# Optimization experiments

Measured on AMD Instinct MI355X. Metric: run time of the kernel, lower is better.

Reference implementation:

```python
import jax, jax.numpy as jnp
import numpy as np

VOCAB = 32000
BLOCK = 2048
C = 1024
H = 16
L = 4
D = C // H
B, T = 1, 2048


def setup_inputs() -> dict:
    key = jax.random.key(0)
    ks = jax.random.split(key, 16)
    s = 0.02
    inp = {
        "input_ids": jax.random.randint(ks[0], (B, T), 0, VOCAB),
        "wte": jax.random.normal(ks[1], (VOCAB, C), jnp.float32) * s,  # tied with lm_head
        "wpe": jax.random.normal(ks[2], (BLOCK, C), jnp.float32) * s,
        "ln1_w": jnp.ones((L, C), jnp.float32),
        "ln1_b": jnp.zeros((L, C), jnp.float32),
        "attn_w": jax.random.normal(ks[3], (L, 3 * C, C), jnp.float32) * s,
        "attn_b": jnp.zeros((L, 3 * C), jnp.float32),
        "proj_w": jax.random.normal(ks[4], (L, C, C), jnp.float32) * (s / np.sqrt(2 * L)),
        "proj_b": jnp.zeros((L, C), jnp.float32),
        "ln2_w": jnp.ones((L, C), jnp.float32),
        "ln2_b": jnp.zeros((L, C), jnp.float32),
        "fc_w": jax.random.normal(ks[5], (L, 4 * C, C), jnp.float32) * s,
        "fc_b": jnp.zeros((L, 4 * C), jnp.float32),
        "fcp_w": jax.random.normal(ks[6], (L, C, 4 * C), jnp.float32) * (s / np.sqrt(2 * L)),
        "fcp_b": jnp.zeros((L, C), jnp.float32),
        "lnf_w": jnp.ones((C,), jnp.float32),
        "lnf_b": jnp.zeros((C,), jnp.float32),
    }
    return inp


def _layernorm(x, w, b, eps=1e-5):
    mu = jnp.mean(x, axis=-1, keepdims=True)
    var = jnp.mean(jnp.square(x - mu), axis=-1, keepdims=True)
    return (x - mu) * jax.lax.rsqrt(var + eps) * w + b


def _block(x, ln1_w, ln1_b, aw, ab, pw, pb, ln2_w, ln2_b, fw, fb, fpw, fpb):
    b, t, c = x.shape
    h = _layernorm(x, ln1_w, ln1_b)
    qkv = h @ aw.T + ab                      # (B,T,3C)
    q, k, v = jnp.split(qkv, 3, axis=-1)
    q = q.reshape(b, t, H, D)
    k = k.reshape(b, t, H, D)
    v = v.reshape(b, t, H, D)
    scale = 1.0 / np.sqrt(D)
    att = jnp.einsum("bqhd,bkhd->bhqk", q, k) * scale   # O(T^2) scores
    mask = jnp.tril(jnp.ones((t, t), bool))
    att = jnp.where(mask, att, -jnp.inf)
    att = jax.nn.softmax(att, axis=-1)
    y = jnp.einsum("bhqk,bkhd->bqhd", att, v).reshape(b, t, c)
    x = x + (y @ pw.T + pb)
    h = _layernorm(x, ln2_w, ln2_b)
    h = jax.nn.gelu(h @ fw.T + fb, approximate=False)
    x = x + (h @ fpw.T + fpb)
    return x


def reference(input_ids, wte, wpe, ln1_w, ln1_b, attn_w, attn_b, proj_w, proj_b,
              ln2_w, ln2_b, fc_w, fc_b, fcp_w, fcp_b, lnf_w, lnf_b):
    b, t = input_ids.shape
    x = wte[input_ids] + wpe[:t]             # (B,T,C)
    for l in range(L):
        x = _block(x, ln1_w[l], ln1_b[l], attn_w[l], attn_b[l], proj_w[l], proj_b[l],
                   ln2_w[l], ln2_b[l], fc_w[l], fc_b[l], fcp_w[l], fcp_b[l])
    x = _layernorm(x, lnf_w, lnf_b)
    logits = x @ wte.T                        # tied lm_head, no bias
    return logits
```

## Files before the change

### kernel.cpp

```cpp
#include <hip/hip_runtime.h>
#include <hip/hip_bf16.h>
#include <math.h>

#define TT 2048
#define CC 1024
#define HH 16
#define DD 64
#define LL 4
#define VOCAB_N 32000

using bf16 = __hip_bfloat16;
typedef __bf16 bf16x8 __attribute__((ext_vector_type(8)));
typedef float f32x4 __attribute__((ext_vector_type(4)));

typedef unsigned int uint_gl __attribute__((address_space(1)));
typedef unsigned int uint_ld __attribute__((address_space(3)));

__device__ __forceinline__ void gload_lds16(const bf16* g, bf16* l) {
    __builtin_amdgcn_global_load_lds((const uint_gl*)g, (uint_ld*)l, 16, 0, 0);
}

__global__ __launch_bounds__(256) void embed_kernel(const int* __restrict__ ids,
                                                    const float* __restrict__ wte,
                                                    const float* __restrict__ wpe,
                                                    float* __restrict__ x) {
    int t = blockIdx.x;
    int id = ids[t];
    int tid = threadIdx.x;
    float4 a = ((const float4*)(wte + (size_t)id * CC))[tid];
    float4 p = ((const float4*)(wpe + (size_t)t * CC))[tid];
    a.x += p.x; a.y += p.y; a.z += p.z; a.w += p.w;
    ((float4*)(x + (size_t)t * CC))[tid] = a;
}

__global__ __launch_bounds__(256) void ln_kernel(const float* __restrict__ x,
                                                 const float* __restrict__ w,
                                                 const float* __restrict__ b,
                                                 bf16* __restrict__ out) {
    int row = blockIdx.x;
    int tid = threadIdx.x;
    const float* xr = x + (size_t)row * CC;
    float4 v = ((const float4*)xr)[tid];
    float s = v.x + v.y + v.z + v.w;
    float ss = v.x * v.x + v.y * v.y + v.z * v.z + v.w * v.w;
    #pragma unroll
    for (int off = 32; off > 0; off >>= 1) {
        s += __shfl_down(s, off, 64);
        ss += __shfl_down(ss, off, 64);
    }
    __shared__ float sbuf[8];
    int wv = tid >> 6;
    if ((tid & 63) == 0) { sbuf[wv] = s; sbuf[4 + wv] = ss; }
    __syncthreads();
    s = sbuf[0] + sbuf[1] + sbuf[2] + sbuf[3];
    ss = sbuf[4] + sbuf[5] + sbuf[6] + sbuf[7];
    float mu = s * (1.0f / CC);
    float var = ss * (1.0f / CC) - mu * mu;
    float rs = rsqrtf(var + 1e-5f);
    float4 wv4 = ((const float4*)w)[tid];
    float4 bv4 = ((const float4*)b)[tid];
    size_t base = (size_t)row * CC + tid * 4;
    out[base + 0] = __float2bfloat16((v.x - mu) * rs * wv4.x + bv4.x);
    out[base + 1] = __float2bfloat16((v.y - mu) * rs * wv4.y + bv4.y);
    out[base + 2] = __float2bfloat16((v.z - mu) * rs * wv4.z + bv4.z);
    out[base + 3] = __float2bfloat16((v.w - mu) * rs * wv4.w + bv4.w);
}

__global__ __launch_bounds__(256) void cvt_kernel(const float* __restrict__ in,
                                                  bf16* __restrict__ out, int n) {
    int i = (blockIdx.x * 256 + threadIdx.x) * 4;
    if (i < n) {
        float4 v = *(const float4*)(in + i);
        out[i + 0] = __float2bfloat16(v.x);
        out[i + 1] = __float2bfloat16(v.y);
        out[i + 2] = __float2bfloat16(v.z);
        out[i + 3] = __float2bfloat16(v.w);
    }
}

template <int EPI, int KSPLIT>
__global__ __launch_bounds__(256) void gemm_bt(const bf16* __restrict__ A,
                                               const bf16* __restrict__ W,
                                               const float* __restrict__ bias,
                                               bf16* __restrict__ outb,
                                               float* __restrict__ outf,
                                               int M, int N, int K) {
    __shared__ bf16 At[128 * 32];
    __shared__ bf16 Bt[128 * 32];
    const int tid = threadIdx.x;
    const int wv = tid >> 6;
    const int ln = tid & 15;
    const int quad = (tid & 63) >> 4;
    const int wm = (wv >> 1) * 64;
    const int wn = (wv & 1) * 64;

    const int gx = gridDim.x, gy = gridDim.y;
    int f = blockIdx.y * gx + blockIdx.x;
    int nfull = gx >> 4;
    int fullB = nfull * 16 * gy;
    int bx, by;
    if (f < fullB) {
        int p = f / (16 * gy);
        int r = f - p * (16 * gy);
        bx = p * 16 + (r & 15);
        by = r >> 4;
    } else {
        int r = f - fullB;
        int w = gx - (nfull << 4);
        bx = (nfull << 4) + r % w;
        by = r / w;
    }
    const int m0 = by * 128;
    const int n0 = bx * 128;
    const int kb = K / KSPLIT;
    const int k_beg = (KSPLIT > 1) ? blockIdx.z * kb : 0;
    const int k_end = k_beg + kb;

    f32x4 acc[4][4];
    #pragma unroll
    for (int i = 0; i < 4; i++)
        #pragma unroll
        for (int j = 0; j < 4; j++)
            #pragma unroll
            for (int r = 0; r < 4; r++) acc[i][j][r] = 0.0f;

    const int rsw = (ln >> 1) & 3;

    for (int k0 = k_beg; k0 < k_end; k0 += 32) {
        #pragma unroll
        for (int r = 0; r < 2; r++) {
            int ci = r * 256 + tid;
            int row = ci >> 2;
            int lc = (ci & 3) ^ ((row >> 1) & 3);
            gload_lds16(A + (size_t)(m0 + row) * K + k0 + lc * 8,
                        At + (size_t)(r * 256 + wv * 64) * 8);
            gload_lds16(W + (size_t)(n0 + row) * K + k0 + lc * 8,
                        Bt + (size_t)(r * 256 + wv * 64) * 8);
        }
        __syncthreads();
        bf16x8 af[4], bfg[4];
        #pragma unroll
        for (int i = 0; i < 4; i++)
            af[i] = *(const bf16x8*)&At[(wm + i * 16 + ln) * 32 + (quad ^ rsw) * 8];
        #pragma unroll
        for (int j = 0; j < 4; j++)
            bfg[j] = *(const bf16x8*)&Bt[(wn + j * 16 + ln) * 32 + (quad ^ rsw) * 8];
        #pragma unroll
        for (int i = 0; i < 4; i++)
            #pragma unroll
            for (int j = 0; j < 4; j++)
                acc[i][j] = __builtin_amdgcn_mfma_f32_16x16x32_bf16(af[i], bfg[j], acc[i][j], 0, 0, 0);
        __syncthreads();
    }

    const bool addBias = (EPI != 3) && (KSPLIT == 1 || blockIdx.z == 0);
    #pragma unroll
    for (int j = 0; j < 4; j++) {
        int col = n0 + wn + j * 16 + ln;
        float bv = addBias ? bias[col] : 0.0f;
        #pragma unroll
        for (int i = 0; i < 4; i++) {
            int rowb = m0 + wm + i * 16 + quad * 4;
            #pragma unroll
            for (int r = 0; r < 4; r++) {
                float v = acc[i][j][r] + bv;
                size_t idx = (size_t)(rowb + r) * N + col;
                if (EPI == 0) {
                    outb[idx] = __float2bfloat16(v);
                } else if (EPI == 1) {
                    outb[idx] = __float2bfloat16(0.5f * v * (1.0f + erff(v * 0.70710678118654752f)));
                } else if (EPI == 2) {
                    if (KSPLIT > 1) atomicAdd(&outf[idx], v);
                    else outf[idx] += v;
                } else {
                    outf[idx] = v;
                }
            }
        }
    }
}

__global__ __launch_bounds__(256) void vtrans_kernel(const bf16* __restrict__ qkv,
                                                     bf16* __restrict__ vT) {
    const int h = blockIdx.x;
    const int t0 = blockIdx.y * 64;
    __shared__ __bf16 tl[64][72];
    const int tid = threadIdx.x;
    const int rhalf = tid >> 3;
    const int c8 = (tid & 7) * 8;
    #pragma unroll
    for (int rr = 0; rr < 2; rr++) {
        int row = rhalf + 32 * rr;
        bf16x8 v = *(const bf16x8*)(qkv + (size_t)(t0 + row) * (3 * CC) + 2 * CC + h * DD + c8);
        #pragma unroll
        for (int i = 0; i < 8; i++) tl[c8 + i][row] = v[i];
    }
    __syncthreads();
    #pragma unroll
    for (int rr = 0; rr < 2; rr++) {
        int d = rhalf + 32 * rr;
        bf16x8 o;
        #pragma unroll
        for (int i = 0; i < 8; i++) o[i] = tl[d][c8 + i];
        *(bf16x8*)(vT + (size_t)(h * DD + d) * TT + t0 + c8) = o;
    }
}

__global__ __launch_bounds__(256) void attn_kernel(const bf16* __restrict__ qkv,
                                                   const bf16* __restrict__ vT,
                                                   bf16* __restrict__ y) {
    const int h = blockIdx.x;
    const int q0 = blockIdx.y * 128;
    const int tid = threadIdx.x;
    const int wq = tid >> 6;
    const int ln = tid & 15;
    const int quad = (tid & 63) >> 4;
    const int wr0 = q0 + wq * 32;

    __shared__ bf16 Kt[64 * 64];
    __shared__ bf16 Vt[64 * 64];
    __shared__ bf16 Pt[4][32 * 72];

    bf16x8 qf[2][2];
    #pragma unroll
    for (int qi = 0; qi < 2; qi++)
        #pragma unroll
        for (int ks = 0; ks < 2; ks++)
            qf[qi][ks] = *(const bf16x8*)(qkv + (size_t)(wr0 + qi * 16 + ln) * (3 * CC) + h * DD + ks * 32 + quad * 8);

    f32x4 oy[2][4];
    float mrow[2], lrow[2];
    #pragma unroll
    for (int i = 0; i < 2; i++) {
        #pragma unroll
        for (int j = 0; j < 4; j++)
            #pragma unroll
            for (int r = 0; r < 4; r++) oy[i][j][r] = 0.0f;
        mrow[i] = -INFINITY;
        lrow[i] = 0.0f;
    }

    const int ntiles = q0 / 64 + 2;
    for (int kt = 0; kt < ntiles; kt++) {
        const int kt0 = kt * 64;
        #pragma unroll
        for (int r = 0; r < 2; r++) {
            int ci = r * 256 + tid;
            int row = ci >> 3;
            int lc = (ci & 7) ^ (row & 7);
            gload_lds16(qkv + (size_t)(kt0 + row) * (3 * CC) + CC + h * DD + lc * 8,
                        Kt + (size_t)(r * 256 + wq * 64) * 8);
            gload_lds16(vT + (size_t)(h * DD + row) * TT + kt0 + lc * 8,
                        Vt + (size_t)(r * 256 + wq * 64) * 8);
        }
        __syncthreads();

        if (kt0 <= wr0) {
            bf16x8 kf[4][2];
            #pragma unroll
            for (int ki = 0; ki < 4; ki++)
                #pragma unroll
                for (int ks = 0; ks < 2; ks++) {
                    int Rk = ki * 16 + ln;
                    kf[ki][ks] = *(const bf16x8*)&Kt[Rk * 64 + (((ks * 4 + quad) ^ (Rk & 7))) * 8];
                }
            f32x4 st[4][2];
            #pragma unroll
            for (int ki = 0; ki < 4; ki++)
                #pragma unroll
                for (int qi = 0; qi < 2; qi++)
                    #pragma unroll
                    for (int r = 0; r < 4; r++) st[ki][qi][r] = 0.0f;
            #pragma unroll
            for (int ks = 0; ks < 2; ks++)
                #pragma unroll
                for (int ki = 0; ki < 4; ki++)
                    #pragma unroll
                    for (int qi = 0; qi < 2; qi++)
                        st[ki][qi] = __builtin_amdgcn_mfma_f32_16x16x32_bf16(kf[ki][ks], qf[qi][ks], st[ki][qi], 0, 0, 0);

            const float scale = 0.125f;
            float alpha[2];
            #pragma unroll
            for (int qi = 0; qi < 2; qi++) {
                int q = wr0 + qi * 16 + ln;
                float sv[4][4];
                float mx = -INFINITY;
                #pragma unroll
                for (int ki = 0; ki < 4; ki++)
                    #pragma unroll
                    for (int r = 0; r < 4; r++) {
                        float t = st[ki][qi][r] * scale;
                        int key = kt0 + ki * 16 + quad * 4 + r;
                        if (key > q) t = -INFINITY;
                        sv[ki][r] = t;
                        mx = fmaxf(mx, t);
                    }
                mx = fmaxf(mx, __shfl_xor(mx, 16, 64));
                mx = fmaxf(mx, __shfl_xor(mx, 32, 64));
                float mnew = fmaxf(mrow[qi], mx);
                alpha[qi] = __expf(mrow[qi] - mnew);
                mrow[qi] = mnew;
                float ps = 0.0f;
                #pragma unroll
                for (int ki = 0; ki < 4; ki++)
                    #pragma unroll
                    for (int r = 0; r < 4; r++) {
                        float p = __expf(sv[ki][r] - mnew);
                        ps += p;
                        Pt[wq][(qi * 16 + ln) * 72 + ki * 16 + quad * 4 + r] = __float2bfloat16(p);
                    }
                ps += __shfl_xor(ps, 16, 64);
                ps += __shfl_xor(ps, 32, 64);
                lrow[qi] = lrow[qi] * alpha[qi] + ps;
            }

            #pragma unroll
            for (int i = 0; i < 2; i++)
                #pragma unroll
                for (int r = 0; r < 4; r++) {
                    float a = __shfl(alpha[i], quad * 4 + r, 16);
                    #pragma unroll
                    for (int dn = 0; dn < 4; dn++) oy[i][dn][r] *= a;
                }

            bf16x8 pf[2][2], vf[4][2];
            #pragma unroll
            for (int i = 0; i < 2; i++)
                #pragma unroll
                for (int ks = 0; ks < 2; ks++)
                    pf[i][ks] = *(const bf16x8*)&Pt[wq][(i * 16 + ln) * 72 + ks * 32 + quad * 8];
            #pragma unroll
            for (int dn = 0; dn < 4; dn++)
                #pragma unroll
                for (int ks = 0; ks < 2; ks++) {
                    int Rd = dn * 16 + ln;
                    vf[dn][ks] = *(const bf16x8*)&Vt[Rd * 64 + (((ks * 4 + quad) ^ (Rd & 7))) * 8];
                }
            #pragma unroll
            for (int ks = 0; ks < 2; ks++)
                #pragma unroll
                for (int i = 0; i < 2; i++)
                    #pragma unroll
                    for (int dn = 0; dn < 4; dn++)
                        oy[i][dn] = __builtin_amdgcn_mfma_f32_16x16x32_bf16(pf[i][ks], vf[dn][ks], oy[i][dn], 0, 0, 0);
        }
        __syncthreads();
    }

    #pragma unroll
    for (int i = 0; i < 2; i++)
        #pragma unroll
        for (int r = 0; r < 4; r++) {
            float linv = 1.0f / __shfl(lrow[i], quad * 4 + r, 16);
            int row = wr0 + i * 16 + quad * 4 + r;
            #pragma unroll
            for (int dn = 0; dn < 4; dn++)
                y[(size_t)row * CC + h * DD + dn * 16 + ln] = __float2bfloat16(oy[i][dn][r] * linv);
        }
}

extern "C" void kernel_launch(void* const* d_in, const int* in_sizes, int n_in,
                              void* d_out, int out_size, void* d_ws, size_t ws_size,
                              hipStream_t stream) {
    const int*   ids    = (const int*)d_in[0];
    const float* wte    = (const float*)d_in[1];
    const float* wpe    = (const float*)d_in[2];
    const float* ln1_w  = (const float*)d_in[3];
    const float* ln1_b  = (const float*)d_in[4];
    const float* attn_w = (const float*)d_in[5];
    const float* attn_b = (const float*)d_in[6];
    const float* proj_w = (const float*)d_in[7];
    const float* proj_b = (const float*)d_in[8];
    const float* ln2_w  = (const float*)d_in[9];
    const float* ln2_b  = (const float*)d_in[10];
    const float* fc_w   = (const float*)d_in[11];
    const float* fc_b   = (const float*)d_in[12];
    const float* fcp_w  = (const float*)d_in[13];
    const float* fcp_b  = (const float*)d_in[14];
    const float* lnf_w  = (const float*)d_in[15];
    const float* lnf_b  = (const float*)d_in[16];

    char* ws = (char*)d_ws;
    float* x    = (float*)(ws);
    bf16* hbuf  = (bf16*)(ws + 8388608);
    bf16* g4buf = (bf16*)(ws + 12582912);
    bf16* qkvb  = (bf16*)(ws + 29360128);
    bf16* ybuf  = (bf16*)(ws + 41943040);
    bf16* wbuf  = (bf16*)(ws + 46137344);
    bf16* vtb   = g4buf;

    embed_kernel<<<TT, 256, 0, stream>>>(ids, wte, wpe, x);

    for (int l = 0; l < LL; l++) {
        ln_kernel<<<TT, 256, 0, stream>>>(x, ln1_w + l * CC, ln1_b + l * CC, hbuf);

        cvt_kernel<<<(3 * CC * CC) / 1024, 256, 0, stream>>>(attn_w + (size_t)l * 3 * CC * CC, wbuf, 3 * CC * CC);
        gemm_bt<0, 1><<<dim3(3 * CC / 128, TT / 128), 256, 0, stream>>>(hbuf, wbuf, attn_b + l * 3 * CC,
                                                                        qkvb, nullptr, TT, 3 * CC, CC);

        vtrans_kernel<<<dim3(HH, TT / 64), 256, 0, stream>>>(qkvb, vtb);
        attn_kernel<<<dim3(HH, TT / 128), 256, 0, stream>>>(qkvb, vtb, ybuf);

        cvt_kernel<<<(CC * CC) / 1024, 256, 0, stream>>>(proj_w + (size_t)l * CC * CC, wbuf, CC * CC);
        gemm_bt<2, 2><<<dim3(CC / 128, TT / 128, 2), 256, 0, stream>>>(ybuf, wbuf, proj_b + l * CC,
                                                                       nullptr, x, TT, CC, CC);

        ln_kernel<<<TT, 256, 0, stream>>>(x, ln2_w + l * CC, ln2_b + l * CC, hbuf);

        cvt_kernel<<<(4 * CC * CC) / 1024, 256, 0, stream>>>(fc_w + (size_t)l * 4 * CC * CC, wbuf, 4 * CC * CC);
        gemm_bt<1, 1><<<dim3(4 * CC / 128, TT / 128), 256, 0, stream>>>(hbuf, wbuf, fc_b + l * 4 * CC,
                                                                        g4buf, nullptr, TT, 4 * CC, CC);

        cvt_kernel<<<(4 * CC * CC) / 1024, 256, 0, stream>>>(fcp_w + (size_t)l * 4 * CC * CC, wbuf, 4 * CC * CC);
        gemm_bt<2, 2><<<dim3(CC / 128, TT / 128, 2), 256, 0, stream>>>(g4buf, wbuf, fcp_b + l * CC,
                                                                       nullptr, x, TT, CC, 4 * CC);
    }

    ln_kernel<<<TT, 256, 0, stream>>>(x, lnf_w, lnf_b, hbuf);
    cvt_kernel<<<(VOCAB_N * CC) / 1024, 256, 0, stream>>>(wte, wbuf, VOCAB_N * CC);
    gemm_bt<3, 1><<<dim3(VOCAB_N / 128, TT / 128), 256, 0, stream>>>(hbuf, wbuf, nullptr,
                                                                     nullptr, (float*)d_out, TT, VOCAB_N, CC);
}
```

Baseline: 1.583 ms.

## Add 256x256 pipelined MFMA GEMM for lm_head and vectorize weight conversion

Replaces the 128x128 GEMM used for the large vocabulary projection with a new 256x256-tile, 512-thread kernel. The new kernel double-buffers LDS via direct global-to-LDS loads with XOR swizzle, interleaves staging with quarter-tile MFMA phases under s_setprio, and remaps workgroups for L2 locality. It also widens the fp32-to-bf16 weight conversion kernel to 8 elements per thread with a single vector store. The larger tiles raise data reuse on the dominant GEMM but use far more LDS and registers, and the hand-written waitcnt/barrier schedule is fragile.

```diff
diff --git a/kernel.cpp b/kernel.cpp
--- a/kernel.cpp
+++ b/kernel.cpp
@@ -19,6 +19,10 @@
 __device__ __forceinline__ void gload_lds16(const bf16* g, bf16* l) {
     __builtin_amdgcn_global_load_lds((const uint_gl*)g, (uint_ld*)l, 16, 0, 0);
 }
+
+#define VMCNT(n) asm volatile("s_waitcnt vmcnt(" #n ")" ::: "memory")
+#define MEMFENCE asm volatile("" ::: "memory")
+#define BAR() do { MEMFENCE; __builtin_amdgcn_s_barrier(); MEMFENCE; } while (0)
 
 __global__ __launch_bounds__(256) void embed_kernel(const int* __restrict__ ids,
                                                     const float* __restrict__ wte,
@@ -68,13 +72,20 @@
 
 __global__ __launch_bounds__(256) void cvt_kernel(const float* __restrict__ in,
                                                   bf16* __restrict__ out, int n) {
-    int i = (blockIdx.x * 256 + threadIdx.x) * 4;
+    int i = (blockIdx.x * 256 + threadIdx.x) * 8;
     if (i < n) {
-        float4 v = *(const float4*)(in + i);
-        out[i + 0] = __float2bfloat16(v.x);
-        out[i + 1] = __float2bfloat16(v.y);
-        out[i + 2] = __float2bfloat16(v.z);
-        out[i + 3] = __float2bfloat16(v.w);
+        float4 a = *(const float4*)(in + i);
+        float4 b = *(const float4*)(in + i + 4);
+        bf16 tmp[8];
+        tmp[0] = __float2bfloat16(a.x);
+        tmp[1] = __float2bfloat16(a.y);
+        tmp[2] = __float2bfloat16(a.z);
+        tmp[3] = __float2bfloat16(a.w);
+        tmp[4] = __float2bfloat16(b.x);
+        tmp[5] = __float2bfloat16(b.y);
+        tmp[6] = __float2bfloat16(b.z);
+        tmp[7] = __float2bfloat16(b.w);
+        *(bf16x8*)(out + i) = *(const bf16x8*)tmp;
     }
 }
 
@@ -178,6 +189,148 @@
             }
         }
     }
+}
+
+__device__ __forceinline__ void stage_q(const bf16* __restrict__ X, bf16* dst,
+                                        int r0, int K, int k0, int q, int tid) {
+    const int g = q * 512 + tid;
+    const int row = g >> 3;
+    const int lc = (g & 7) ^ (row & 7);
+    gload_lds16(X + (size_t)(r0 + row) * K + k0 + lc * 8,
+                dst + (size_t)(q * 512 + (tid & 0x1C0)) * 8);
+}
+
+template <int QI>
+__device__ __forceinline__ void rd_a(const bf16* Ab, int wm2, int ln, int quad, bf16x8 af[4][2]) {
+    #pragma unroll
+    for (int i = 0; i < 4; i++) {
+        const int row = wm2 * 128 + QI * 64 + i * 16 + ln;
+        #pragma unroll
+        for (int ks = 0; ks < 2; ks++)
+            af[i][ks] = *(const bf16x8*)&Ab[row * 64 + ((ks * 4 + quad) ^ (ln & 7)) * 8];
+    }
+}
+
+template <int QJ>
+__device__ __forceinline__ void rd_b(const bf16* Bb, int wn2, int ln, int quad, bf16x8 bfr[2][2]) {
+    #pragma unroll
+    for (int j = 0; j < 2; j++) {
+        const int row = wn2 * 64 + QJ * 32 + j * 16 + ln;
+        #pragma unroll
+        for (int ks = 0; ks < 2; ks++)
+            bfr[j][ks] = *(const bf16x8*)&Bb[row * 64 + ((ks * 4 + quad) ^ (ln & 7)) * 8];
+    }
+}
+
+template <int QI, int QJ>
+__device__ __forceinline__ void mfma_q(bf16x8 af[4][2], bf16x8 bfr[2][2], f32x4 acc[8][4]) {
+    __builtin_amdgcn_s_setprio(1);
+    #pragma unroll
+    for (int ks = 0; ks < 2; ks++)
+        #pragma unroll
+        for (int i = 0; i < 4; i++)
+            #pragma unroll
+            for (int j = 0; j < 2; j++)
+                acc[QI * 4 + i][QJ * 2 + j] =
+                    __builtin_amdgcn_mfma_f32_16x16x32_bf16(af[i][ks], bfr[j][ks],
+                                                            acc[QI * 4 + i][QJ * 2 + j], 0, 0, 0);
+    __builtin_amdgcn_s_setprio(0);
+}
+
+__global__ __launch_bounds__(512, 2) void gemm256(const bf16* __restrict__ A,
+                                                  const bf16* __restrict__ W,
+                                                  float* __restrict__ out,
+                                                  int M, int N, int K) {
+    __shared__ bf16 As[2][256 * 64];
+    __shared__ bf16 Bs[2][256 * 64];
+    const int tid = threadIdx.x;
+    const int ln = tid & 15;
+    const int quad = (tid & 63) >> 4;
+    const int wv = tid >> 6;
+    const int wm2 = wv >> 2;
+    const int wn2 = wv & 3;
+
+    const int cpx = gridDim.x >> 3;
+    const int wg = (blockIdx.x & 7) * cpx + (blockIdx.x >> 3);
+    const int byn = M >> 8;
+    const int bx = wg / byn;
+    const int by = wg - bx * byn;
+    const int m0 = by * 256;
+    const int n0 = bx * 256;
+
+    f32x4 acc[8][4];
+    #pragma unroll
+    for (int i = 0; i < 8; i++)
+        #pragma unroll
+        for (int j = 0; j < 4; j++)
+            #pragma unroll
+            for (int r = 0; r < 4; r++) acc[i][j][r] = 0.0f;
+
+    const int nt = K >> 6;
+
+    #pragma unroll
+    for (int q = 0; q < 4; q++) stage_q(A, As[0], m0, K, 0, q, tid);
+    #pragma unroll
+    for (int q = 0; q < 4; q++) stage_q(W, Bs[0], n0, K, 0, q, tid);
+    #pragma unroll
+    for (int q = 0; q < 4; q++) stage_q(A, As[1], m0, K, 64, q, tid);
+
+    for (int tt = 0; tt < nt; tt++) {
+        const int c = tt & 1;
+        const bf16* Ab = As[c];
+        const bf16* Bb = Bs[c];
+        bf16* An = As[c];
+        bf16* Bn = Bs[c ^ 1];
+
+        if (tt < nt - 1) { VMCNT(4); } else { VMCNT(0); }
+        __builtin_amdgcn_s_barrier();
+        MEMFENCE;
+
+        bf16x8 af[4][2], bfr[2][2];
+
+        if (tt + 1 < nt) {
+            #pragma unroll
+            for (int q = 0; q < 4; q++) stage_q(W, Bn, n0, K, (tt + 1) * 64, q, tid);
+        }
+        rd_a<0>(Ab, wm2, ln, quad, af);
+        rd_b<0>(Bb, wn2, ln, quad, bfr);
+        BAR();
+        mfma_q<0, 0>(af, bfr, acc);
+        BAR();
+
+        if (tt + 2 < nt) {
+            stage_q(A, An, m0, K, (tt + 2) * 64, 0, tid);
+            stage_q(A, An, m0, K, (tt + 2) * 64, 2, tid);
+        }
+        rd_b<1>(Bb, wn2, ln, quad, bfr);
+        BAR();
+        mfma_q<0, 1>(af, bfr, acc);
+        BAR();
+
+        rd_a<1>(Ab, wm2, ln, quad, af);
+        BAR();
+        mfma_q<1, 1>(af, bfr, acc);
+        BAR();
+
+        if (tt + 2 < nt) {
+            stage_q(A, An, m0, K, (tt + 2) * 64, 1, tid);
+            stage_q(A, An, m0, K, (tt + 2) * 64, 3, tid);
+        }
+        rd_b<0>(Bb, wn2, ln, quad, bfr);
+        BAR();
+        mfma_q<1, 0>(af, bfr, acc);
+    }
+
+    #pragma unroll
+    for (int gi = 0; gi < 8; gi++)
+        #pragma unroll
+        for (int gj = 0; gj < 4; gj++) {
+            const int rowb = m0 + wm2 * 128 + gi * 16 + quad * 4;
+            const int col = n0 + wn2 * 64 + gj * 16 + ln;
+            #pragma unroll
+            for (int r = 0; r < 4; r++)
+                out[(size_t)(rowb + r) * N + col] = acc[gi][gj][r];
+        }
 }
 
 __global__ __launch_bounds__(256) void vtrans_kernel(const bf16* __restrict__ qkv,
@@ -395,30 +548,30 @@
     for (int l = 0; l < LL; l++) {
         ln_kernel<<<TT, 256, 0, stream>>>(x, ln1_w + l * CC, ln1_b + l * CC, hbuf);
 
-        cvt_kernel<<<(3 * CC * CC) / 1024, 256, 0, stream>>>(attn_w + (size_t)l * 3 * CC * CC, wbuf, 3 * CC * CC);
+        cvt_kernel<<<(3 * CC * CC) / 2048, 256, 0, stream>>>(attn_w + (size_t)l * 3 * CC * CC, wbuf, 3 * CC * CC);
         gemm_bt<0, 1><<<dim3(3 * CC / 128, TT / 128), 256, 0, stream>>>(hbuf, wbuf, attn_b + l * 3 * CC,
                                                                         qkvb, nullptr, TT, 3 * CC, CC);
 
         vtrans_kernel<<<dim3(HH, TT / 64), 256, 0, stream>>>(qkvb, vtb);
         attn_kernel<<<dim3(HH, TT / 128), 256, 0, stream>>>(qkvb, vtb, ybuf);
 
-        cvt_kernel<<<(CC * CC) / 1024, 256, 0, stream>>>(proj_w + (size_t)l * CC * CC, wbuf, CC * CC);
+        cvt_kernel<<<(CC * CC) / 2048, 256, 0, stream>>>(proj_w + (size_t)l * CC * CC, wbuf, CC * CC);
         gemm_bt<2, 2><<<dim3(CC / 128, TT / 128, 2), 256, 0, stream>>>(ybuf, wbuf, proj_b + l * CC,
                                                                        nullptr, x, TT, CC, CC);
 
         ln_kernel<<<TT, 256, 0, stream>>>(x, ln2_w + l * CC, ln2_b + l * CC, hbuf);
 
-        cvt_kernel<<<(4 * CC * CC) / 1024, 256, 0, stream>>>(fc_w + (size_t)l * 4 * CC * CC, wbuf, 4 * CC * CC);
+        cvt_kernel<<<(4 * CC * CC) / 2048, 256, 0, stream>>>(fc_w + (size_t)l * 4 * CC * CC, wbuf, 4 * CC * CC);
         gemm_bt<1, 1><<<dim3(4 * CC / 128, TT / 128), 256, 0, stream>>>(hbuf, wbuf, fc_b + l * 4 * CC,
                                                                         g4buf, nullptr, TT, 4 * CC, CC);
 
-        cvt_kernel<<<(4 * CC * CC) / 1024, 256, 0, stream>>>(fcp_w + (size_t)l * 4 * CC * CC, wbuf, 4 * CC * CC);
+        cvt_kernel<<<(4 * CC * CC) / 2048, 256, 0, stream>>>(fcp_w + (size_t)l * 4 * CC * CC, wbuf, 4 * CC * CC);
         gemm_bt<2, 2><<<dim3(CC / 128, TT / 128, 2), 256, 0, stream>>>(g4buf, wbuf, fcp_b + l * CC,
                                                                        nullptr, x, TT, CC, 4 * CC);
     }
 
     ln_kernel<<<TT, 256, 0, stream>>>(x, lnf_w, lnf_b, hbuf);
-    cvt_kernel<<<(VOCAB_N * CC) / 1024, 256, 0, stream>>>(wte, wbuf, VOCAB_N * CC);
-    gemm_bt<3, 1><<<dim3(VOCAB_N / 128, TT / 128), 256, 0, stream>>>(hbuf, wbuf, nullptr,
-                                                                     nullptr, (float*)d_out, TT, VOCAB_N, CC);
-}
+    cvt_kernel<<<(VOCAB_N * CC) / 2048, 256, 0, stream>>>(wte, wbuf, VOCAB_N * CC);
+    gemm256<<<dim3((VOCAB_N / 256) * (TT / 256)), 512, 0, stream>>>(hbuf, wbuf, (float*)d_out,
+                                                                    TT, VOCAB_N, CC);
+}
```

Measured after the change: 1.567 ms. No clear change (-1.0%).
